# Kernel optimization log

Measured on AMD Instinct MI355X. Metric: run time of the kernel, lower is better.

Reference implementation:

```python
import jax, jax.numpy as jnp
import numpy as np


def _prelu(x, a):
    # nn.PReLU() with a single learnable parameter a
    return jnp.where(x >= 0, x, a * x)


def _conv1x1(x, w, b):
    # x: [n, cin, h, w], w: [cout, cin], b: [cout]
    return jnp.einsum('nchw,oc->nohw', x, w) + b[None, :, None, None]


def setup_inputs() -> dict:
    key = jax.random.key(0)
    ks = jax.random.split(key, 7)
    N, C, H, W = 8, 64, 64, 64
    red = 2
    c = C // red
    s = 1.0 / np.sqrt(C).astype(np.float32)
    x = jax.random.normal(ks[0], (N, C, H, W), dtype=jnp.float32)
    w1 = jax.random.normal(ks[1], (c, C), dtype=jnp.float32) * s
    b1 = jnp.zeros((c,), dtype=jnp.float32)
    w2 = jax.random.normal(ks[2], (c, C), dtype=jnp.float32) * s
    b2 = jnp.zeros((c,), dtype=jnp.float32)
    w3 = jax.random.normal(ks[3], (C, C), dtype=jnp.float32) * s
    b3 = jnp.zeros((C,), dtype=jnp.float32)
    a1 = jnp.full((1,), 0.25, dtype=jnp.float32)
    a2 = jnp.full((1,), 0.25, dtype=jnp.float32)
    a3 = jnp.full((1,), 0.25, dtype=jnp.float32)
    return {"x": x, "w1": w1, "b1": b1, "a1": a1, "w2": w2, "b2": b2,
            "a2": a2, "w3": w3, "b3": b3, "a3": a3}


def reference(x, w1, b1, a1, w2, b2, a2, w3, b3, a3):
    res_scale = 1.0
    n, C, h, w = x.shape
    e1 = _prelu(_conv1x1(x, w1, b1), a1[0])  # [n, c, h, w]
    e2 = _prelu(_conv1x1(x, w2, b2), a2[0])  # [n, c, h, w]
    e3 = _prelu(_conv1x1(x, w3, b3), a3[0])  # [n, C, h, w]
    c = e1.shape[1]
    hw = h * w
    q = e1.transpose(0, 2, 3, 1).reshape(n, hw, c)   # [n, hw, c]
    k = e2.reshape(n, c, hw)                         # [n, c, hw]
    score = jax.nn.softmax(jnp.matmul(q, k), axis=-1)  # [n, hw, hw]
    v = e3.reshape(n, C, hw).transpose(0, 2, 1)      # [n, hw, C]
    out = jnp.matmul(score, v)                       # [n, hw, C]
    out = out.transpose(0, 2, 1).reshape(n, C, h, w)
    return out + res_scale * x
```

## Files before the change

kernel.cpp:

```cpp
#include <hip/hip_runtime.h>
#include <hip/hip_bf16.h>

typedef __bf16 bf16x8 __attribute__((ext_vector_type(8)));
typedef float  f32x4  __attribute__((ext_vector_type(4)));
typedef float  f32x16 __attribute__((ext_vector_type(16)));
typedef int    i32x4  __attribute__((ext_vector_type(4)));

#define SEQ 4096
#define CIN 64
#define KBLK 64
#define KSPLIT 4
#define KCHUNK (SEQ / KSPLIT)
#define NTC (KCHUNK / KBLK)
#define LOG2E 1.44269504088896340736f

__device__ __forceinline__ void gll16(const void* g, void* l) {
    __builtin_amdgcn_global_load_lds(
        (const __attribute__((address_space(1))) void*)g,
        (__attribute__((address_space(3))) void*)l, 16, 0, 0);
}

__device__ __forceinline__ unsigned cvtpk(float lo, float hi) {
    unsigned r;
    asm("v_cvt_pk_bf16_f32 %0, %1, %2" : "=v"(r) : "v"(lo), "v"(hi));
    return r;
}

__global__ __launch_bounds__(256, 2) void qkv_gen(
    const float* __restrict__ x,
    const float* __restrict__ w1, const float* __restrict__ b1, const float* __restrict__ a1,
    const float* __restrict__ w2, const float* __restrict__ b2, const float* __restrict__ a2,
    const float* __restrict__ w3, const float* __restrict__ b3, const float* __restrict__ a3,
    __bf16* __restrict__ qws, __bf16* __restrict__ kws, __bf16* __restrict__ vtws)
{
    __shared__ float xs[CIN][64];
    __shared__ float wl[CIN][128];
    __shared__ float bl[128];
    __shared__ float al[4];

    const int t  = threadIdx.x;
    const int n  = blockIdx.x >> 6;
    const int p0 = (blockIdx.x & 63) << 6;

    for (int idx = t; idx < 2048; idx += 256) {
        int j = idx >> 6, c = idx & 63;
        wl[c][j]      = w1[idx];
        wl[c][32 + j] = w2[idx];
    }
    for (int idx = t; idx < 4096; idx += 256) {
        int j = idx >> 6, c = idx & 63;
        wl[c][64 + j] = w3[idx];
    }
    if (t < 32) { bl[t] = b1[t]; bl[32 + t] = b2[t]; }
    if (t >= 128 && t < 192) bl[64 + (t - 128)] = b3[t - 128];
    if (t == 0) { al[0] = a1[0]; al[1] = a2[0]; al[2] = a3[0]; }

    const float* xb = x + ((size_t)n * CIN) * SEQ + p0;
    for (int r = 0; r < 16; ++r) {
        int e = r * 256 + t;
        xs[e >> 6][e & 63] = xb[(size_t)(e >> 6) * SEQ + (e & 63)];
    }
    __syncthreads();

    const int p  = t & 63;
    const int g  = t >> 6;
    const int jb = g << 5;
    const float a = (g == 0) ? al[0] : ((g == 1) ? al[1] : al[2]);

    float acc[32];
    #pragma unroll
    for (int j = 0; j < 32; ++j) acc[j] = bl[jb + j];

    for (int c = 0; c < CIN; ++c) {
        float xv = xs[c][p];
        const f32x4* wr = (const f32x4*)&wl[c][jb];
        #pragma unroll
        for (int j4 = 0; j4 < 8; ++j4) {
            f32x4 wv = wr[j4];
            acc[j4*4+0] = fmaf(wv[0], xv, acc[j4*4+0]);
            acc[j4*4+1] = fmaf(wv[1], xv, acc[j4*4+1]);
            acc[j4*4+2] = fmaf(wv[2], xv, acc[j4*4+2]);
            acc[j4*4+3] = fmaf(wv[3], xv, acc[j4*4+3]);
        }
    }
    #pragma unroll
    for (int j = 0; j < 32; ++j) acc[j] = acc[j] >= 0.f ? acc[j] : a * acc[j];

    const int pg = p0 + p;
    if (g <= 1) {
        const float sc = (g == 0) ? LOG2E : 1.0f;
        __bf16* dst = (g == 0 ? qws : kws) + ((size_t)n * SEQ + pg) * 32;
        #pragma unroll
        for (int v8 = 0; v8 < 4; ++v8) {
            bf16x8 o;
            #pragma unroll
            for (int i = 0; i < 8; ++i) o[i] = (__bf16)(acc[v8*8+i] * sc);
            *(bf16x8*)(dst + v8*8) = o;
        }
    } else {
        __bf16* dst = vtws + ((size_t)n * CIN + (jb - 64)) * SEQ + pg;
        #pragma unroll
        for (int j = 0; j < 32; ++j) dst[(size_t)j * SEQ] = (__bf16)acc[j];
    }
}

__global__ __launch_bounds__(256, 4) void attn(
    const __bf16* __restrict__ qws, const __bf16* __restrict__ kws,
    const __bf16* __restrict__ vtws,
    float* __restrict__ Ows, float* __restrict__ lws)
{
    __shared__ __align__(16) char stg[3][12288];

    const int t    = threadIdx.x;
    const int lane = t & 63;
    const int n    = blockIdx.x & 7;
    const int qblk = (blockIdx.x >> 3) & 31;
    const int ks   = blockIdx.x >> 8;
    const int wid  = t >> 6;
    const int l31  = lane & 31;
    const int h    = lane >> 5;
    const int qbase = qblk * 128 + wid * 32;
    const int kbase = ks * KCHUNK;
    const int ksw  = ((l31 >> 1) & 3) << 4;
    const int vsw  = (l31 & 7) << 4;

    const char* kb = (const char*)(kws + (size_t)n * SEQ * 32);
    const char* vb = (const char*)(vtws + (size_t)n * CIN * SEQ);

    const char* qp = (const char*)(qws + (size_t)n * SEQ * 32)
                     + (size_t)(qbase + l31) * 64 + h * 16;
    const bf16x8 qf0 = *(const bf16x8*)(qp);
    const bf16x8 qf1 = *(const bf16x8*)(qp + 32);

    f32x16 of0 = {}, of1 = {};
    float ls = 0.f;

    auto stage = [&](int k0n, int b) {
        {
            int row = t >> 2;
            int c16 = (t & 3) ^ ((t >> 3) & 3);
            gll16(kb + (size_t)(k0n + row) * 64 + c16 * 16, &stg[b][0] + t * 16);
        }
        #pragma unroll
        for (int j = 0; j < 2; ++j) {
            int L   = j * 4096 + t * 16;
            int row = j * 32 + (t >> 3);
            int c16 = (t & 7) ^ ((t >> 3) & 7);
            gll16(vb + (size_t)row * 8192 + (size_t)k0n * 2 + c16 * 16,
                  &stg[b][4096] + L);
        }
    };

    stage(kbase, 0);
    stage(kbase + KBLK, 1);

    int cur = 0;
    for (int tt = 0; tt < NTC; ++tt) {
        if (tt + 1 < NTC) {
            asm volatile("s_waitcnt vmcnt(3)" ::: "memory");
        } else {
            asm volatile("s_waitcnt vmcnt(0)" ::: "memory");
        }
        __builtin_amdgcn_s_barrier();

        if (tt + 2 < NTC) {
            int nb = cur + 2; if (nb >= 3) nb -= 3;
            stage(kbase + (tt + 2) * KBLK, nb);
        }

        const char* kc_ = &stg[cur][0];
        const char* vc_ = &stg[cur][4096];

        unsigned c0[8], c1[8];

        #pragma unroll
        for (int kti = 0; kti < 2; ++kti) {
            const char* krow = kc_ + (size_t)(kti * 32 + l31) * 64;
            bf16x8 kf0 = *(const bf16x8*)(krow + ((h * 16) ^ ksw));
            bf16x8 kf1 = *(const bf16x8*)(krow + ((32 + h * 16) ^ ksw));
            f32x16 s = {};
            __builtin_amdgcn_s_setprio(1);
            s = __builtin_amdgcn_mfma_f32_32x32x16_bf16(kf0, qf0, s, 0, 0, 0);
            s = __builtin_amdgcn_mfma_f32_32x32x16_bf16(kf1, qf1, s, 0, 0, 0);
            __builtin_amdgcn_s_setprio(0);

            float p[16];
            #pragma unroll
            for (int r = 0; r < 16; ++r) {
                p[r] = __builtin_exp2f(s[r]);
                ls += p[r];
            }
            unsigned* c = kti ? c1 : c0;
            #pragma unroll
            for (int j = 0; j < 4; ++j) {
                c[j]     = cvtpk(p[2*j],     p[2*j + 1]);
                c[4 + j] = cvtpk(p[8 + 2*j], p[9 + 2*j]);
            }
            asm("v_permlane32_swap_b32 %0, %1" : "+v"(c[0]), "+v"(c[2]));
            asm("v_permlane32_swap_b32 %0, %1" : "+v"(c[1]), "+v"(c[3]));
            asm("v_permlane32_swap_b32 %0, %1" : "+v"(c[4]), "+v"(c[6]));
            asm("v_permlane32_swap_b32 %0, %1" : "+v"(c[5]), "+v"(c[7]));
        }

        __builtin_amdgcn_s_setprio(1);
        #pragma unroll
        for (int s4 = 0; s4 < 4; ++s4) {
            const unsigned* cs = (s4 < 2) ? c0 : c1;
            const int sl = (s4 & 1) * 4;
            i32x4 bi = { (int)cs[sl], (int)cs[sl+1], (int)cs[sl+2], (int)cs[sl+3] };
            bf16x8 pf = __builtin_bit_cast(bf16x8, bi);
            const int colv = (s4 * 32 + h * 16) ^ vsw;
            bf16x8 vf0 = *(const bf16x8*)(vc_ + (size_t)l31 * 128 + colv);
            bf16x8 vf1 = *(const bf16x8*)(vc_ + (size_t)(32 + l31) * 128 + colv);
            of0 = __builtin_amdgcn_mfma_f32_32x32x16_bf16(vf0, pf, of0, 0, 0, 0);
            of1 = __builtin_amdgcn_mfma_f32_32x32x16_bf16(vf1, pf, of1, 0, 0, 0);
        }
        __builtin_amdgcn_s_setprio(0);

        cur = (cur == 2) ? 0 : cur + 1;
    }

    const int qg = qbase + l31;
    float* Ob = Ows + (size_t)n * CIN * SEQ;
    #pragma unroll
    for (int r = 0; r < 16; ++r) {
        int dv = (r & 3) + 8 * (r >> 2) + 4 * h;
        unsafeAtomicAdd(Ob + (size_t)dv * SEQ + qg,        of0[r]);
        unsafeAtomicAdd(Ob + (size_t)(dv + 32) * SEQ + qg, of1[r]);
    }
    unsafeAtomicAdd(lws + n * SEQ + qg, ls);
}

__global__ __launch_bounds__(256) void combine(
    const float* __restrict__ Ows, const float* __restrict__ lws,
    const float* __restrict__ x, float* __restrict__ out)
{
    const int total = 8 * CIN * SEQ / 4;
    for (int i = blockIdx.x * 256 + threadIdx.x; i < total; i += gridDim.x * 256) {
        int q4 = i & (SEQ / 4 - 1);
        int nd = i >> 10;
        int n  = nd >> 6;
        f32x4 o4 = *(const f32x4*)(Ows + (size_t)i * 4);
        f32x4 l4 = *(const f32x4*)(lws + (size_t)n * SEQ + q4 * 4);
        f32x4 x4 = *(const f32x4*)(x + (size_t)i * 4);
        f32x4 r;
        r[0] = o4[0] / l4[0] + x4[0];
        r[1] = o4[1] / l4[1] + x4[1];
        r[2] = o4[2] / l4[2] + x4[2];
        r[3] = o4[3] / l4[3] + x4[3];
        *(f32x4*)(out + (size_t)i * 4) = r;
    }
}

extern "C" void kernel_launch(void* const* d_in, const int* in_sizes, int n_in,
                              void* d_out, int out_size, void* d_ws, size_t ws_size,
                              hipStream_t stream)
{
    (void)in_sizes; (void)n_in; (void)out_size; (void)ws_size;
    const float* x  = (const float*)d_in[0];
    const float* w1 = (const float*)d_in[1];
    const float* b1 = (const float*)d_in[2];
    const float* a1 = (const float*)d_in[3];
    const float* w2 = (const float*)d_in[4];
    const float* b2 = (const float*)d_in[5];
    const float* a2 = (const float*)d_in[6];
    const float* w3 = (const float*)d_in[7];
    const float* b3 = (const float*)d_in[8];
    const float* a3 = (const float*)d_in[9];
    float* out = (float*)d_out;

    char* ws = (char*)d_ws;
    __bf16* qws  = (__bf16*)(ws);
    __bf16* kws  = (__bf16*)(ws + (2u << 20));
    __bf16* vtws = (__bf16*)(ws + (4u << 20));
    float*  Ows  = (float*)(ws + (8u << 20));
    float*  lws  = (float*)(ws + (16u << 20));

    hipMemsetAsync(Ows, 0, (8u << 20) + (128u << 10), stream);
    hipLaunchKernelGGL(qkv_gen, dim3(512), dim3(256), 0, stream,
                       x, w1, b1, a1, w2, b2, a2, w3, b3, a3, qws, kws, vtws);
    hipLaunchKernelGGL(attn, dim3(8 * 32 * KSPLIT), dim3(256), 0, stream,
                       qws, kws, vtws, Ows, lws);
    hipLaunchKernelGGL(combine, dim3(1024), dim3(256), 0, stream,
                       Ows, lws, x, out);
}
```

Measured before the change: 90.94 us.

## Write per-split bf16 partials instead of atomics, double KSPLIT, shrink LDS buffering

Doubles the key split to 8 so the attention grid holds more blocks. When the workspace is large enough, each split writes its bf16 partial output and row-sum to its own slice instead of doing float atomics, so the memset goes away. A new reduction kernel inverts the summed row sums, and a new combine kernel adds the 8 partials and the residual. Staging drops from triple to double buffering, with a full vmcnt wait each step, to allow 6 blocks per CU. The cost is more partial-output traffic, an extra launch, and bf16 rounding of the partials.

```diff
diff --git a/kernel.cpp b/kernel.cpp
--- a/kernel.cpp
+++ b/kernel.cpp
@@ -9,7 +9,7 @@
 #define SEQ 4096
 #define CIN 64
 #define KBLK 64
-#define KSPLIT 4
+#define KSPLIT 8
 #define KCHUNK (SEQ / KSPLIT)
 #define NTC (KCHUNK / KBLK)
 #define LOG2E 1.44269504088896340736f
@@ -104,12 +104,13 @@
     }
 }
 
-__global__ __launch_bounds__(256, 4) void attn(
+template<int ATOMIC>
+__global__ __launch_bounds__(256, 6) void attn(
     const __bf16* __restrict__ qws, const __bf16* __restrict__ kws,
     const __bf16* __restrict__ vtws,
-    float* __restrict__ Ows, float* __restrict__ lws)
-{
-    __shared__ __align__(16) char stg[3][12288];
+    void* __restrict__ Ows, float* __restrict__ lws)
+{
+    __shared__ __align__(16) char stg[2][12288];
 
     const int t    = threadIdx.x;
     const int lane = t & 63;
@@ -152,21 +153,13 @@
     };
 
     stage(kbase, 0);
-    stage(kbase + KBLK, 1);
 
     int cur = 0;
     for (int tt = 0; tt < NTC; ++tt) {
-        if (tt + 1 < NTC) {
-            asm volatile("s_waitcnt vmcnt(3)" ::: "memory");
-        } else {
-            asm volatile("s_waitcnt vmcnt(0)" ::: "memory");
-        }
+        asm volatile("s_waitcnt vmcnt(0)" ::: "memory");
         __builtin_amdgcn_s_barrier();
 
-        if (tt + 2 < NTC) {
-            int nb = cur + 2; if (nb >= 3) nb -= 3;
-            stage(kbase + (tt + 2) * KBLK, nb);
-        }
+        if (tt + 1 < NTC) stage(kbase + (tt + 1) * KBLK, cur ^ 1);
 
         const char* kc_ = &stg[cur][0];
         const char* vc_ = &stg[cur][4096];
@@ -217,29 +210,82 @@
         }
         __builtin_amdgcn_s_setprio(0);
 
-        cur = (cur == 2) ? 0 : cur + 1;
+        cur ^= 1;
     }
 
     const int qg = qbase + l31;
-    float* Ob = Ows + (size_t)n * CIN * SEQ;
+    if (ATOMIC) {
+        float* Ob = (float*)Ows + (size_t)n * CIN * SEQ;
+        #pragma unroll
+        for (int r = 0; r < 16; ++r) {
+            int dv = (r & 3) + 8 * (r >> 2) + 4 * h;
+            unsafeAtomicAdd(Ob + (size_t)dv * SEQ + qg,        of0[r]);
+            unsafeAtomicAdd(Ob + (size_t)(dv + 32) * SEQ + qg, of1[r]);
+        }
+        unsafeAtomicAdd(lws + n * SEQ + qg, ls);
+    } else {
+        __bf16* Ob = (__bf16*)Ows + (size_t)ks * (8 * CIN * SEQ) + (size_t)n * CIN * SEQ;
+        #pragma unroll
+        for (int r = 0; r < 16; ++r) {
+            int dv = (r & 3) + 8 * (r >> 2) + 4 * h;
+            Ob[(size_t)dv * SEQ + qg]        = (__bf16)of0[r];
+            Ob[(size_t)(dv + 32) * SEQ + qg] = (__bf16)of1[r];
+        }
+        float lt = ls + __shfl_xor(ls, 32);
+        if (h == 0) lws[(size_t)ks * (8 * SEQ) + n * SEQ + qg] = lt;
+    }
+}
+
+__global__ __launch_bounds__(256) void lred(float* __restrict__ lws)
+{
+    int i = blockIdx.x * 256 + threadIdx.x;
+    float s = 0.f;
     #pragma unroll
-    for (int r = 0; r < 16; ++r) {
-        int dv = (r & 3) + 8 * (r >> 2) + 4 * h;
-        unsafeAtomicAdd(Ob + (size_t)dv * SEQ + qg,        of0[r]);
-        unsafeAtomicAdd(Ob + (size_t)(dv + 32) * SEQ + qg, of1[r]);
-    }
-    unsafeAtomicAdd(lws + n * SEQ + qg, ls);
-}
-
-__global__ __launch_bounds__(256) void combine(
+    for (int ks = 0; ks < KSPLIT; ++ks) s += lws[ks * 32768 + i];
+    lws[i] = 1.f / s;
+}
+
+__global__ __launch_bounds__(256) void combine8(
+    const __bf16* __restrict__ O8, const float* __restrict__ linv,
+    const float* __restrict__ x, float* __restrict__ out)
+{
+    const int i = blockIdx.x * 256 + threadIdx.x;
+    const int q8 = i & 511;
+    const int nd = i >> 9;
+    const int n  = nd >> 6;
+
+    float o[8] = {};
+    const __bf16* base = O8 + (size_t)nd * SEQ + q8 * 8;
+    #pragma unroll
+    for (int ks = 0; ks < KSPLIT; ++ks) {
+        bf16x8 v = *(const bf16x8*)(base + (size_t)ks * (8 * CIN * SEQ));
+        #pragma unroll
+        for (int j = 0; j < 8; ++j) o[j] += (float)v[j];
+    }
+    const float* ivp = linv + n * SEQ + q8 * 8;
+    f32x4 iv0 = *(const f32x4*)(ivp);
+    f32x4 iv1 = *(const f32x4*)(ivp + 4);
+    const float* xp = x + (size_t)nd * SEQ + q8 * 8;
+    f32x4 x0 = *(const f32x4*)(xp);
+    f32x4 x1 = *(const f32x4*)(xp + 4);
+    f32x4 r0, r1;
+    r0[0] = o[0]*iv0[0] + x0[0]; r0[1] = o[1]*iv0[1] + x0[1];
+    r0[2] = o[2]*iv0[2] + x0[2]; r0[3] = o[3]*iv0[3] + x0[3];
+    r1[0] = o[4]*iv1[0] + x1[0]; r1[1] = o[5]*iv1[1] + x1[1];
+    r1[2] = o[6]*iv1[2] + x1[2]; r1[3] = o[7]*iv1[3] + x1[3];
+    float* op = out + (size_t)nd * SEQ + q8 * 8;
+    *(f32x4*)(op)     = r0;
+    *(f32x4*)(op + 4) = r1;
+}
+
+__global__ __launch_bounds__(256) void combine1(
     const float* __restrict__ Ows, const float* __restrict__ lws,
     const float* __restrict__ x, float* __restrict__ out)
 {
     const int total = 8 * CIN * SEQ / 4;
     for (int i = blockIdx.x * 256 + threadIdx.x; i < total; i += gridDim.x * 256) {
-        int q4 = i & (SEQ / 4 - 1);
-        int nd = i >> 10;
-        int n  = nd >> 6;
+        int q4 = i & 1023;
+        int n  = i >> 16;
         f32x4 o4 = *(const f32x4*)(Ows + (size_t)i * 4);
         f32x4 l4 = *(const f32x4*)(lws + (size_t)n * SEQ + q4 * 4);
         f32x4 x4 = *(const f32x4*)(x + (size_t)i * 4);
@@ -256,7 +302,7 @@
                               void* d_out, int out_size, void* d_ws, size_t ws_size,
                               hipStream_t stream)
 {
-    (void)in_sizes; (void)n_in; (void)out_size; (void)ws_size;
+    (void)in_sizes; (void)n_in; (void)out_size;
     const float* x  = (const float*)d_in[0];
     const float* w1 = (const float*)d_in[1];
     const float* b1 = (const float*)d_in[2];
@@ -273,14 +319,26 @@
     __bf16* qws  = (__bf16*)(ws);
     __bf16* kws  = (__bf16*)(ws + (2u << 20));
     __bf16* vtws = (__bf16*)(ws + (4u << 20));
-    float*  Ows  = (float*)(ws + (8u << 20));
-    float*  lws  = (float*)(ws + (16u << 20));
-
-    hipMemsetAsync(Ows, 0, (8u << 20) + (128u << 10), stream);
+
     hipLaunchKernelGGL(qkv_gen, dim3(512), dim3(256), 0, stream,
                        x, w1, b1, a1, w2, b2, a2, w3, b3, a3, qws, kws, vtws);
-    hipLaunchKernelGGL(attn, dim3(8 * 32 * KSPLIT), dim3(256), 0, stream,
-                       qws, kws, vtws, Ows, lws);
-    hipLaunchKernelGGL(combine, dim3(1024), dim3(256), 0, stream,
-                       Ows, lws, x, out);
-}
+
+    const size_t need_split = (8u << 20) + (32u << 20) + (1u << 20);
+    if (ws_size >= need_split) {
+        __bf16* O8   = (__bf16*)(ws + (8u << 20));
+        float*  lws8 = (float*)(ws + (40u << 20));
+        hipLaunchKernelGGL(attn<0>, dim3(8 * 32 * KSPLIT), dim3(256), 0, stream,
+                           qws, kws, vtws, (void*)O8, lws8);
+        hipLaunchKernelGGL(lred, dim3(128), dim3(256), 0, stream, lws8);
+        hipLaunchKernelGGL(combine8, dim3(1024), dim3(256), 0, stream,
+                           O8, lws8, x, out);
+    } else {
+        float* Ows = (float*)(ws + (8u << 20));
+        float* lws = (float*)(ws + (16u << 20));
+        hipMemsetAsync(Ows, 0, (8u << 20) + (128u << 10), stream);
+        hipLaunchKernelGGL(attn<1>, dim3(8 * 32 * KSPLIT), dim3(256), 0, stream,
+                           qws, kws, vtws, (void*)Ows, lws);
+        hipLaunchKernelGGL(combine1, dim3(1024), dim3(256), 0, stream,
+                           Ows, lws, x, out);
+    }
+}
```

Result: slower. 246.6 us (+171.2%).
